# Kernel optimization log

Hardware: AMD Instinct MI355X
Metric: run time of the kernel (lower is better)

Reference implementation:

```python
import jax, jax.numpy as jnp
import numpy as np

EMB = 16
N_LEFT = 100000
N_RIGHT = 100000
N_EDGES = 3200000


def setup_inputs() -> dict:
    key = jax.random.key(0)
    ks = jax.random.split(key, 16)
    s = 1.0 / np.sqrt(EMB)
    inp = {
        "left_features": jax.random.normal(ks[0], (N_LEFT, EMB), jnp.float32),
        "edge_indices": jax.random.randint(ks[1], (2, N_EDGES), 0, N_RIGHT, jnp.int64) if jax.config.jax_enable_x64 else jax.random.randint(ks[1], (2, N_EDGES), 0, N_RIGHT, jnp.int32),
        "edge_features": jax.random.normal(ks[2], (N_EDGES, 1), jnp.float32),
        "right_features": jax.random.normal(ks[3], (N_RIGHT, EMB), jnp.float32),
        # feature_module_left: Linear(emb, emb, bias=True)
        "W_left": jax.random.uniform(ks[4], (EMB, EMB), jnp.float32, -s, s),
        "b_left": jax.random.uniform(ks[5], (EMB,), jnp.float32, -s, s),
        # feature_module_edge: Linear(1, emb, bias=False)
        "W_edge": jax.random.uniform(ks[6], (1, EMB), jnp.float32, -1.0, 1.0),
        # feature_module_right: Linear(emb, emb, bias=False)
        "W_right": jax.random.uniform(ks[7], (EMB, EMB), jnp.float32, -s, s),
        # feature_module_final: ReLU -> Linear(emb, emb)
        "W_final": jax.random.uniform(ks[8], (EMB, EMB), jnp.float32, -s, s),
        "b_final": jax.random.uniform(ks[9], (EMB,), jnp.float32, -s, s),
        # post_conv_module: ReLU -> Linear(emb, emb)
        "W_post": jax.random.uniform(ks[10], (EMB, EMB), jnp.float32, -s, s),
        "b_post": jax.random.uniform(ks[11], (EMB,), jnp.float32, -s, s),
        # output_module: Linear(2*emb, emb) -> ReLU -> Linear(emb, emb)
        "W_out1": jax.random.uniform(ks[12], (2 * EMB, EMB), jnp.float32, -1.0 / np.sqrt(2 * EMB), 1.0 / np.sqrt(2 * EMB)),
        "b_out1": jax.random.uniform(ks[13], (EMB,), jnp.float32, -s, s),
        "W_out2": jax.random.uniform(ks[14], (EMB, EMB), jnp.float32, -s, s),
        "b_out2": jax.random.uniform(ks[15], (EMB,), jnp.float32, -s, s),
    }
    return inp


def reference(left_features, edge_indices, edge_features, right_features,
              W_left, b_left, W_edge, W_right, W_final, b_final,
              W_post, b_post, W_out1, b_out1, W_out2, b_out2):
    left_idx = edge_indices[0]
    right_idx = edge_indices[1]
    n_right = right_features.shape[0]

    # per-edge messages: [E, emb]
    msg_left = left_features[left_idx] @ W_left + b_left
    msg_edge = edge_features @ W_edge
    msg_right = right_features[right_idx] @ W_right
    messages = jax.nn.relu(msg_left + msg_edge + msg_right) @ W_final + b_final

    # scatter-add over right nodes
    aggregated = jax.ops.segment_sum(messages, right_idx, num_segments=n_right)

    post = jax.nn.relu(aggregated) @ W_post + b_post
    h = jnp.concatenate([post, right_features], axis=-1)  # [N_right, 2*emb]
    out = jax.nn.relu(h @ W_out1 + b_out1) @ W_out2 + b_out2
    return out
```

## Files before the change

kernel.cpp:

```cpp
#include <hip/hip_runtime.h>

#define EMB 16
#define NPB 196
#define BNODES 256
#define MAXNB 512
#define PCHUNK 6656
#define RPTC 13
#define MAXCHUNKS 512
#define REC_CAP 2048
#define RPT 4
typedef unsigned int u32;
typedef unsigned long long u64;

__global__ void zero_f32(float* __restrict__ p, size_t n) {
    size_t i = (size_t)blockIdx.x * blockDim.x + threadIdx.x;
    size_t stride = (size_t)gridDim.x * blockDim.x;
    for (; i < n; i += stride) p[i] = 0.0f;
}

__global__ void zero_i32(int* __restrict__ p, int n) {
    int i = blockIdx.x * blockDim.x + threadIdx.x;
    if (i < n) p[i] = 0;
}

__device__ __forceinline__ u32 bf16bits_rne(float x) {
    u32 u = __float_as_uint(x);
    return (u + 0x7fffu + ((u >> 16) & 1u)) >> 16;
}

__global__ void linear16_pack_kernel(const float* __restrict__ X, const float* __restrict__ W,
                                     const float* __restrict__ b, u32* __restrict__ Y, int N) {
    int tid = blockIdx.x * blockDim.x + threadIdx.x;
    int row = tid >> 3;
    int h = tid & 7;
    if (row >= N) return;
    float a0 = b ? b[h] : 0.0f;
    float a1 = b ? b[h + 8] : 0.0f;
    const float* xr = X + (size_t)row * EMB;
#pragma unroll
    for (int k = 0; k < EMB; ++k) {
        float xv = xr[k];
        a0 = fmaf(xv, W[k * EMB + h], a0);
        a1 = fmaf(xv, W[k * EMB + h + 8], a1);
    }
    Y[(size_t)row * 8 + h] = (bf16bits_rne(a1) << 16) | bf16bits_rne(a0);
}

__global__ void linear16_kernel(const float* __restrict__ X, const float* __restrict__ W,
                                const float* __restrict__ b, float* __restrict__ Y, int N) {
    int tid = blockIdx.x * blockDim.x + threadIdx.x;
    int row = tid >> 4;
    int j = tid & 15;
    if (row >= N) return;
    float acc = b ? b[j] : 0.0f;
    const float* xr = X + (size_t)row * EMB;
#pragma unroll
    for (int k = 0; k < EMB; ++k) acc = fmaf(xr[k], W[k * EMB + j], acc);
    Y[(size_t)row * EMB + j] = acc;
}

__launch_bounds__(512)
__global__ void chunk_sort_kernel(const int* __restrict__ eidx, const float* __restrict__ ef,
                                  u64* __restrict__ rec, int* __restrict__ cntM,
                                  int* __restrict__ cbaseM, int E, int NB) {
    __shared__ u64 srec[PCHUNK];
    __shared__ int hist[MAXNB];
    __shared__ int sc[512];
    int t = threadIdx.x;
    int c = blockIdx.x;
    long long base = (long long)c * PCHUNK;
    int n = (int)(((long long)E - base) < PCHUNK ? ((long long)E - base) : PCHUNK);
    const int* ridx = eidx + E;

    for (int i = t; i < NB; i += 512) hist[i] = 0;
    __syncthreads();
    int rank[RPTC];
#pragma unroll
    for (int k = 0; k < RPTC; ++k) {
        int i = t + k * 512;
        rank[k] = (i < n) ? atomicAdd(&hist[ridx[base + i] / NPB], 1) : 0;
    }
    __syncthreads();
    int v = (t < NB) ? hist[t] : 0;
    sc[t] = v;
    __syncthreads();
    for (int d = 1; d < 512; d <<= 1) {
        int x = (t >= d) ? sc[t - d] : 0;
        __syncthreads();
        sc[t] += x;
        __syncthreads();
    }
    int ex = sc[t] - v;
    if (t < NB) {
        cntM[(size_t)c * NB + t] = v;
        cbaseM[(size_t)c * NB + t] = ex;
        hist[t] = ex;
    }
    __syncthreads();
#pragma unroll
    for (int k = 0; k < RPTC; ++k) {
        int i = t + k * 512;
        if (i < n) {
            int r = ridx[base + i];
            int bb = r / NPB;
            int rl = r - bb * NPB;
            int l = eidx[base + i];
            float f = ef[base + i];
            int pos = hist[bb] + rank[k];
            srec[pos] = ((u64)__float_as_uint(f) << 32) | ((u64)(u32)l << 8) | (u32)rl;
        }
    }
    __syncthreads();
    for (int i = t; i < n; i += 512) rec[base + i] = srec[i];
}

__launch_bounds__(512)
__global__ void bucket_gather_kernel(const u64* __restrict__ rec, const int* __restrict__ cntM,
                                     const int* __restrict__ cbaseM,
                                     const u32* __restrict__ Lpk, const u32* __restrict__ Rpk,
                                     const float* __restrict__ We,
                                     float* __restrict__ S, int* __restrict__ deg,
                                     int n_right, int NB, int nchunks) {
    __shared__ u64 srec[REC_CAP];
    __shared__ u32 addrtab[REC_CAP];
    __shared__ int runsum[MAXCHUNKS + 1];
    __shared__ int rbase[MAXCHUNKS];
    __shared__ int ssc[512];
    __shared__ int hist[BNODES], base_[BNODES];
    int b = blockIdx.x;
    int t = threadIdx.x;
    int node0 = b * NPB;

    int len = (t < nchunks) ? cntM[(size_t)t * NB + b] : 0;
    ssc[t] = len;
    __syncthreads();
    for (int d = 1; d < 512; d <<= 1) {
        int x = (t >= d) ? ssc[t - d] : 0;
        __syncthreads();
        ssc[t] += x;
        __syncthreads();
    }
    int pexcl = ssc[t] - len;
    if (t < nchunks) { runsum[t] = pexcl; rbase[t] = t * PCHUNK + cbaseM[(size_t)t * NB + b]; }
    if (t == 511) runsum[nchunks] = ssc[511];
    __syncthreads();
    int total = runsum[nchunks];

    int n = t >> 1, q = t & 1;
    int node = node0 + n;
    bool nv = (n < NPB) && (node < n_right);

    float we[16];
#pragma unroll
    for (int j = 0; j < 16; ++j) we[j] = We[j];

    float rv[16];
    if (nv) {
        const uint4* rp = (const uint4*)(Rpk + (size_t)node * 8);
        uint4 ra = rp[0], rb = rp[1];
        u32 w0 = ra.x, w1 = ra.y, w2 = ra.z, w3 = ra.w;
        u32 w4 = rb.x, w5 = rb.y, w6 = rb.z, w7 = rb.w;
        rv[0] = __uint_as_float(w0 << 16); rv[8]  = __uint_as_float(w0 & 0xffff0000u);
        rv[1] = __uint_as_float(w1 << 16); rv[9]  = __uint_as_float(w1 & 0xffff0000u);
        rv[2] = __uint_as_float(w2 << 16); rv[10] = __uint_as_float(w2 & 0xffff0000u);
        rv[3] = __uint_as_float(w3 << 16); rv[11] = __uint_as_float(w3 & 0xffff0000u);
        rv[4] = __uint_as_float(w4 << 16); rv[12] = __uint_as_float(w4 & 0xffff0000u);
        rv[5] = __uint_as_float(w5 << 16); rv[13] = __uint_as_float(w5 & 0xffff0000u);
        rv[6] = __uint_as_float(w6 << 16); rv[14] = __uint_as_float(w6 & 0xffff0000u);
        rv[7] = __uint_as_float(w7 << 16); rv[15] = __uint_as_float(w7 & 0xffff0000u);
    } else {
#pragma unroll
        for (int j = 0; j < 16; ++j) rv[j] = 0.0f;
    }

    float acc[16];
#pragma unroll
    for (int j = 0; j < 16; ++j) acc[j] = 0.0f;
    int dsum = 0;

    for (int tile0 = 0; tile0 < total; tile0 += REC_CAP) {
        int m = total - tile0; if (m > REC_CAP) m = REC_CAP;
        u64 rcl[RPT];
        int rnk[RPT];
        if (t < BNODES) hist[t] = 0;
        for (int r = t; r < nchunks; r += 512) {
            int g_lo = runsum[r], g_hi = runsum[r + 1];
            int lo = g_lo > tile0 ? g_lo : tile0;
            int hi = g_hi < tile0 + m ? g_hi : tile0 + m;
            int a = rbase[r] + (lo - g_lo);
            for (int g = lo; g < hi; ++g, ++a) addrtab[g - tile0] = (u32)a;
        }
        __syncthreads();
#pragma unroll
        for (int k = 0; k < RPT; ++k) {
            int i = t + k * 512;
            rcl[k] = (i < m) ? rec[(size_t)addrtab[i]] : 0;
        }
#pragma unroll
        for (int k = 0; k < RPT; ++k) {
            int i = t + k * 512;
            rnk[k] = (i < m) ? atomicAdd(&hist[(int)(rcl[k] & 0xffu)], 1) : 0;
        }
        __syncthreads();
        if (t < 64) {
            int h0 = hist[4 * t], h1 = hist[4 * t + 1], h2 = hist[4 * t + 2], h3 = hist[4 * t + 3];
            int s4 = h0 + h1 + h2 + h3;
            int inc = s4;
#pragma unroll
            for (int d = 1; d < 64; d <<= 1) {
                int x = __shfl_up(inc, d, 64);
                if (t >= d) inc += x;
            }
            int ex = inc - s4;
            base_[4 * t] = ex;
            base_[4 * t + 1] = ex + h0;
            base_[4 * t + 2] = ex + h0 + h1;
            base_[4 * t + 3] = ex + h0 + h1 + h2;
        }
        __syncthreads();
#pragma unroll
        for (int k = 0; k < RPT; ++k) {
            int i = t + k * 512;
            if (i < m) srec[base_[(int)(rcl[k] & 0xffu)] + rnk[k]] = rcl[k];
        }
        __syncthreads();
        {
            int cc = nv ? hist[n] : 0;
            int b0_ = nv ? base_[n] : 0;
            if (q == 0) dsum += cc;
            for (int k = q; k < cc; k += 2) {
                u64 rc = srec[b0_ + k];
                int l = (int)((rc >> 8) & 0xFFFFFFu);
                float f = __uint_as_float((u32)(rc >> 32));
                const uint4* lp = (const uint4*)(Lpk + (size_t)l * 8);
                uint4 la = lp[0], lb = lp[1];
                u32 w0 = la.x, w1 = la.y, w2 = la.z, w3 = la.w;
                u32 w4 = lb.x, w5 = lb.y, w6 = lb.z, w7 = lb.w;
#define PAIR(h, lw) { \
                float l0 = __uint_as_float(lw << 16); \
                float l1 = __uint_as_float(lw & 0xffff0000u); \
                acc[h]     += fmaxf(fmaf(f, we[h], l0) + rv[h], 0.0f); \
                acc[h + 8] += fmaxf(fmaf(f, we[h + 8], l1) + rv[h + 8], 0.0f); }
                PAIR(0, w0) PAIR(1, w1) PAIR(2, w2) PAIR(3, w3)
                PAIR(4, w4) PAIR(5, w5) PAIR(6, w6) PAIR(7, w7)
#undef PAIR
            }
        }
        __syncthreads();
    }

#pragma unroll
    for (int j = 0; j < 16; ++j) acc[j] += __shfl_xor(acc[j], 1, 64);
    if (nv) {
        float4* Op = (float4*)(S + (size_t)node * EMB);
        Op[q * 2]     = make_float4(acc[q * 8],     acc[q * 8 + 1], acc[q * 8 + 2], acc[q * 8 + 3]);
        Op[q * 2 + 1] = make_float4(acc[q * 8 + 4], acc[q * 8 + 5], acc[q * 8 + 6], acc[q * 8 + 7]);
        if (q == 0) deg[node] = dsum;
    }
}

__global__ void edge_kernel(const int* __restrict__ eidx, const float* __restrict__ ef,
                            const float* __restrict__ L, const float* __restrict__ R,
                            const float* __restrict__ We, float* __restrict__ S,
                            int* __restrict__ cnt, int E) {
    long long tid = (long long)blockIdx.x * blockDim.x + threadIdx.x;
    int e = (int)(tid >> 4);
    int j = (int)(tid & 15);
    if (e >= E) return;
    int l = eidx[e];
    int r = eidx[E + e];
    float v = L[(size_t)l * EMB + j] + ef[e] * We[j] + R[(size_t)r * EMB + j];
    v = fmaxf(v, 0.0f);
    unsafeAtomicAdd(&S[(size_t)r * EMB + j], v);
    if (j == 0) atomicAdd(&cnt[r], 1);
}

__global__ void final_kernel(const float* __restrict__ S, const int* __restrict__ deg,
                             const float* __restrict__ rf,
                             const float* __restrict__ Wf, const float* __restrict__ bf,
                             const float* __restrict__ Wp, const float* __restrict__ bp,
                             const float* __restrict__ Wo1, const float* __restrict__ bo1,
                             const float* __restrict__ Wo2, const float* __restrict__ bo2,
                             float* __restrict__ out, int N) {
    __shared__ float sWf[256], sWp[256], sWo1[512], sWo2[256];
    __shared__ float sb[64];
    int t = threadIdx.x;
    for (int i = t; i < 256; i += 256) { sWf[i] = Wf[i]; sWp[i] = Wp[i]; sWo2[i] = Wo2[i]; }
    for (int i = t; i < 512; i += 256) sWo1[i] = Wo1[i];
    if (t < 16) { sb[t] = bf[t]; sb[16 + t] = bp[t]; sb[32 + t] = bo1[t]; sb[48 + t] = bo2[t]; }
    __syncthreads();

    int r = blockIdx.x * blockDim.x + t;
    if (r >= N) return;

    float s[16], x[16], y[16], rv[16], z[16], o[16];
    const float4* Sp = (const float4*)(S + (size_t)r * EMB);
    const float4* Rp = (const float4*)(rf + (size_t)r * EMB);
#pragma unroll
    for (int k = 0; k < 4; ++k) {
        float4 v = Sp[k];
        s[4 * k] = v.x; s[4 * k + 1] = v.y; s[4 * k + 2] = v.z; s[4 * k + 3] = v.w;
        float4 w = Rp[k];
        rv[4 * k] = w.x; rv[4 * k + 1] = w.y; rv[4 * k + 2] = w.z; rv[4 * k + 3] = w.w;
    }
    float c = (float)deg[r];

#pragma unroll
    for (int j = 0; j < 16; ++j) {
        float a = c * sb[j];
#pragma unroll
        for (int k = 0; k < 16; ++k) a = fmaf(s[k], sWf[k * 16 + j], a);
        x[j] = fmaxf(a, 0.0f);
    }
#pragma unroll
    for (int j = 0; j < 16; ++j) {
        float a = sb[16 + j];
#pragma unroll
        for (int k = 0; k < 16; ++k) a = fmaf(x[k], sWp[k * 16 + j], a);
        y[j] = a;
    }
#pragma unroll
    for (int j = 0; j < 16; ++j) {
        float a = sb[32 + j];
#pragma unroll
        for (int k = 0; k < 16; ++k) a = fmaf(y[k], sWo1[k * 16 + j], a);
#pragma unroll
        for (int k = 0; k < 16; ++k) a = fmaf(rv[k], sWo1[(16 + k) * 16 + j], a);
        z[j] = fmaxf(a, 0.0f);
    }
#pragma unroll
    for (int j = 0; j < 16; ++j) {
        float a = sb[48 + j];
#pragma unroll
        for (int k = 0; k < 16; ++k) a = fmaf(z[k], sWo2[k * 16 + j], a);
        o[j] = a;
    }
    float4* Op = (float4*)(out + (size_t)r * EMB);
#pragma unroll
    for (int k = 0; k < 4; ++k)
        Op[k] = make_float4(o[4 * k], o[4 * k + 1], o[4 * k + 2], o[4 * k + 3]);
}

extern "C" void kernel_launch(void* const* d_in, const int* in_sizes, int n_in,
                              void* d_out, int out_size, void* d_ws, size_t ws_size,
                              hipStream_t stream) {
    const float* lf     = (const float*)d_in[0];
    const int*   eidx   = (const int*)d_in[1];
    const float* ef     = (const float*)d_in[2];
    const float* rf     = (const float*)d_in[3];
    const float* W_left = (const float*)d_in[4];
    const float* b_left = (const float*)d_in[5];
    const float* W_edge = (const float*)d_in[6];
    const float* W_right= (const float*)d_in[7];
    const float* W_final= (const float*)d_in[8];
    const float* b_final= (const float*)d_in[9];
    const float* W_post = (const float*)d_in[10];
    const float* b_post = (const float*)d_in[11];
    const float* W_out1 = (const float*)d_in[12];
    const float* b_out1 = (const float*)d_in[13];
    const float* W_out2 = (const float*)d_in[14];
    const float* b_out2 = (const float*)d_in[15];

    int n_left  = in_sizes[0] / EMB;
    int E       = in_sizes[2];
    int n_right = in_sizes[3] / EMB;
    float* out = (float*)d_out;

    int NB = (n_right + NPB - 1) / NPB;
    int nchunks = (E + PCHUNK - 1) / PCHUNK;

    size_t need = (size_t)E * 8
                + (size_t)nchunks * NB * 8
                + ((size_t)n_left + n_right) * 32
                + (size_t)n_right * EMB * 4
                + (size_t)n_right * 4;

    if (ws_size >= need && NB <= MAXNB && nchunks <= MAXCHUNKS) {
        u64* rec    = (u64*)d_ws;
        int* cntM   = (int*)(rec + (size_t)E);
        int* cbaseM = cntM + (size_t)nchunks * NB;
        u32* Lpk    = (u32*)(cbaseM + (size_t)nchunks * NB);
        u32* Rpk    = Lpk + (size_t)n_left * 8;
        float* S    = (float*)(Rpk + (size_t)n_right * 8);
        int* deg    = (int*)(S + (size_t)n_right * EMB);

        linear16_pack_kernel<<<(n_left * 8 + 255) / 256, 256, 0, stream>>>(lf, W_left, b_left, Lpk, n_left);
        linear16_pack_kernel<<<(n_right * 8 + 255) / 256, 256, 0, stream>>>(rf, W_right, nullptr, Rpk, n_right);

        chunk_sort_kernel<<<nchunks, 512, 0, stream>>>(eidx, ef, rec, cntM, cbaseM, E, NB);

        bucket_gather_kernel<<<NB, 512, 0, stream>>>(rec, cntM, cbaseM, Lpk, Rpk, W_edge,
                                                     S, deg, n_right, NB, nchunks);

        final_kernel<<<(n_right + 255) / 256, 256, 0, stream>>>(S, deg, rf,
            W_final, b_final, W_post, b_post, W_out1, b_out1, W_out2, b_out2, out, n_right);
    } else {
        float* L   = (float*)d_ws;
        float* R   = L + (size_t)n_left * EMB;
        float* S   = R + (size_t)n_right * EMB;
        int*   cnt = (int*)(S + (size_t)n_right * EMB);

        zero_f32<<<2048, 256, 0, stream>>>(S, (size_t)n_right * EMB);
        zero_i32<<<(n_right + 255) / 256, 256, 0, stream>>>(cnt, n_right);

        linear16_kernel<<<(n_left * EMB + 255) / 256, 256, 0, stream>>>(lf, W_left, b_left, L, n_left);
        linear16_kernel<<<(n_right * EMB + 255) / 256, 256, 0, stream>>>(rf, W_right, nullptr, R, n_right);

        long long ethreads = (long long)E * EMB;
        edge_kernel<<<(unsigned)((ethreads + 255) / 256), 256, 0, stream>>>(eidx, ef, L, R, W_edge, S, cnt, E);

        final_kernel<<<(n_right + 255) / 256, 256, 0, stream>>>(S, cnt, rf,
            W_final, b_final, W_post, b_post, W_out1, b_out1, W_out2, b_out2, out, n_right);
    }
}
```

Measured before the change: 91.77 us.

## Fuse final MLP into bucket gather and keep sort records in registers

The per-node output MLP (final linear, post linear, output two-layer MLP) moves into the tail of bucket_gather_kernel, with weights staged in shared memory. This removes the separate final_kernel launch and the round-trip of the aggregated S and deg arrays through global memory. In chunk_sort_kernel, each edge's packed record and bucket/rank are now built in the first pass and held in registers, so edge indices and features are not re-read from global memory in the scatter pass. The cost is higher register pressure in both kernels, and both lanes of each node pair now compute the full 16x16 MLP chain redundantly.

Result: faster. 87.75 us (-4.4%).

```diff
diff --git a/kernel.cpp b/kernel.cpp
--- a/kernel.cpp
+++ b/kernel.cpp
@@ -74,11 +74,22 @@
 
     for (int i = t; i < NB; i += 512) hist[i] = 0;
     __syncthreads();
-    int rank[RPTC];
+    u64 rcv[RPTC];
+    int pk[RPTC];
 #pragma unroll
     for (int k = 0; k < RPTC; ++k) {
         int i = t + k * 512;
-        rank[k] = (i < n) ? atomicAdd(&hist[ridx[base + i] / NPB], 1) : 0;
+        rcv[k] = 0; pk[k] = 0;
+        if (i < n) {
+            int r = ridx[base + i];
+            int l = eidx[base + i];
+            float f = ef[base + i];
+            int bb = r / NPB;
+            int rl = r - bb * NPB;
+            int rank = atomicAdd(&hist[bb], 1);
+            rcv[k] = ((u64)__float_as_uint(f) << 32) | ((u64)(u32)l << 8) | (u32)rl;
+            pk[k] = (bb << 13) | rank;
+        }
     }
     __syncthreads();
     int v = (t < NB) ? hist[t] : 0;
@@ -100,15 +111,7 @@
 #pragma unroll
     for (int k = 0; k < RPTC; ++k) {
         int i = t + k * 512;
-        if (i < n) {
-            int r = ridx[base + i];
-            int bb = r / NPB;
-            int rl = r - bb * NPB;
-            int l = eidx[base + i];
-            float f = ef[base + i];
-            int pos = hist[bb] + rank[k];
-            srec[pos] = ((u64)__float_as_uint(f) << 32) | ((u64)(u32)l << 8) | (u32)rl;
-        }
+        if (i < n) srec[hist[pk[k] >> 13] + (pk[k] & 8191)] = rcv[k];
     }
     __syncthreads();
     for (int i = t; i < n; i += 512) rec[base + i] = srec[i];
@@ -118,8 +121,12 @@
 __global__ void bucket_gather_kernel(const u64* __restrict__ rec, const int* __restrict__ cntM,
                                      const int* __restrict__ cbaseM,
                                      const u32* __restrict__ Lpk, const u32* __restrict__ Rpk,
-                                     const float* __restrict__ We,
-                                     float* __restrict__ S, int* __restrict__ deg,
+                                     const float* __restrict__ We, const float* __restrict__ rf,
+                                     const float* __restrict__ Wf, const float* __restrict__ bf,
+                                     const float* __restrict__ Wp, const float* __restrict__ bp,
+                                     const float* __restrict__ Wo1, const float* __restrict__ bo1,
+                                     const float* __restrict__ Wo2, const float* __restrict__ bo2,
+                                     float* __restrict__ out,
                                      int n_right, int NB, int nchunks) {
     __shared__ u64 srec[REC_CAP];
     __shared__ u32 addrtab[REC_CAP];
@@ -127,9 +134,14 @@
     __shared__ int rbase[MAXCHUNKS];
     __shared__ int ssc[512];
     __shared__ int hist[BNODES], base_[BNODES];
+    __shared__ float sWf[256], sWp[256], sWo1[512], sWo2[256], sb[64];
     int b = blockIdx.x;
     int t = threadIdx.x;
     int node0 = b * NPB;
+
+    if (t < 256) { sWf[t] = Wf[t]; sWp[t] = Wp[t]; sWo2[t] = Wo2[t]; }
+    sWo1[t] = Wo1[t];
+    if (t < 16) { sb[t] = bf[t]; sb[16 + t] = bp[t]; sb[32 + t] = bo1[t]; sb[48 + t] = bo2[t]; }
 
     int len = (t < nchunks) ? cntM[(size_t)t * NB + b] : 0;
     ssc[t] = len;
@@ -251,11 +263,51 @@
 
 #pragma unroll
     for (int j = 0; j < 16; ++j) acc[j] += __shfl_xor(acc[j], 1, 64);
+    dsum += __shfl_xor(dsum, 1, 64);
+
     if (nv) {
-        float4* Op = (float4*)(S + (size_t)node * EMB);
-        Op[q * 2]     = make_float4(acc[q * 8],     acc[q * 8 + 1], acc[q * 8 + 2], acc[q * 8 + 3]);
-        Op[q * 2 + 1] = make_float4(acc[q * 8 + 4], acc[q * 8 + 5], acc[q * 8 + 6], acc[q * 8 + 7]);
-        if (q == 0) deg[node] = dsum;
+        float rfx[16];
+        const float4* Rf = (const float4*)(rf + (size_t)node * EMB);
+#pragma unroll
+        for (int k = 0; k < 4; ++k) {
+            float4 w = Rf[k];
+            rfx[4 * k] = w.x; rfx[4 * k + 1] = w.y; rfx[4 * k + 2] = w.z; rfx[4 * k + 3] = w.w;
+        }
+        float c = (float)dsum;
+        float x[16], y[16], z[16], o[16];
+#pragma unroll
+        for (int j = 0; j < 16; ++j) {
+            float a = c * sb[j];
+#pragma unroll
+            for (int k = 0; k < 16; ++k) a = fmaf(acc[k], sWf[k * 16 + j], a);
+            x[j] = fmaxf(a, 0.0f);
+        }
+#pragma unroll
+        for (int j = 0; j < 16; ++j) {
+            float a = sb[16 + j];
+#pragma unroll
+            for (int k = 0; k < 16; ++k) a = fmaf(x[k], sWp[k * 16 + j], a);
+            y[j] = a;
+        }
+#pragma unroll
+        for (int j = 0; j < 16; ++j) {
+            float a = sb[32 + j];
+#pragma unroll
+            for (int k = 0; k < 16; ++k) a = fmaf(y[k], sWo1[k * 16 + j], a);
+#pragma unroll
+            for (int k = 0; k < 16; ++k) a = fmaf(rfx[k], sWo1[(16 + k) * 16 + j], a);
+            z[j] = fmaxf(a, 0.0f);
+        }
+#pragma unroll
+        for (int j = 0; j < 16; ++j) {
+            float a = sb[48 + j];
+#pragma unroll
+            for (int k = 0; k < 16; ++k) a = fmaf(z[k], sWo2[k * 16 + j], a);
+            o[j] = a;
+        }
+        float4* Op = (float4*)(out + (size_t)node * EMB);
+        Op[q * 2]     = make_float4(o[q * 8],     o[q * 8 + 1], o[q * 8 + 2], o[q * 8 + 3]);
+        Op[q * 2 + 1] = make_float4(o[q * 8 + 4], o[q * 8 + 5], o[q * 8 + 6], o[q * 8 + 7]);
     }
 }
 
@@ -371,9 +423,7 @@
 
     size_t need = (size_t)E * 8
                 + (size_t)nchunks * NB * 8
-                + ((size_t)n_left + n_right) * 32
-                + (size_t)n_right * EMB * 4
-                + (size_t)n_right * 4;
+                + ((size_t)n_left + n_right) * 32;
 
     if (ws_size >= need && NB <= MAXNB && nchunks <= MAXCHUNKS) {
         u64* rec    = (u64*)d_ws;
@@ -381,19 +431,16 @@
         int* cbaseM = cntM + (size_t)nchunks * NB;
         u32* Lpk    = (u32*)(cbaseM + (size_t)nchunks * NB);
         u32* Rpk    = Lpk + (size_t)n_left * 8;
-        float* S    = (float*)(Rpk + (size_t)n_right * 8);
-        int* deg    = (int*)(S + (size_t)n_right * EMB);
 
         linear16_pack_kernel<<<(n_left * 8 + 255) / 256, 256, 0, stream>>>(lf, W_left, b_left, Lpk, n_left);
         linear16_pack_kernel<<<(n_right * 8 + 255) / 256, 256, 0, stream>>>(rf, W_right, nullptr, Rpk, n_right);
 
         chunk_sort_kernel<<<nchunks, 512, 0, stream>>>(eidx, ef, rec, cntM, cbaseM, E, NB);
 
-        bucket_gather_kernel<<<NB, 512, 0, stream>>>(rec, cntM, cbaseM, Lpk, Rpk, W_edge,
-                                                     S, deg, n_right, NB, nchunks);
-
-        final_kernel<<<(n_right + 255) / 256, 256, 0, stream>>>(S, deg, rf,
-            W_final, b_final, W_post, b_post, W_out1, b_out1, W_out2, b_out2, out, n_right);
+        bucket_gather_kernel<<<NB, 512, 0, stream>>>(rec, cntM, cbaseM, Lpk, Rpk, W_edge, rf,
+                                                     W_final, b_final, W_post, b_post,
+                                                     W_out1, b_out1, W_out2, b_out2,
+                                                     out, n_right, NB, nchunks);
     } else {
         float* L   = (float*)d_ws;
         float* R   = L + (size_t)n_left * EMB;
```
